# Optimization experiments

Measured on AMD Instinct MI355X. Metric: run time of the kernel, lower is better.

## Reference

```python
import jax, jax.numpy as jnp
import numpy as np

WS = 8      # window_size
NH = 8      # n_heads
EPS = 1e-06


def _rel_coords(ws):
    # Swin-style relative position index table, matches torch buffer construction
    c = np.stack(np.meshgrid(np.arange(ws), np.arange(ws), indexing='ij'))  # [2,ws,ws]
    c = c.reshape(2, -1)                      # [2, L]
    rel = c[:, :, None] - c[:, None, :]       # [2, L, L]
    rel = rel.transpose(1, 2, 0) + (ws - 1)   # [L, L, 2]
    rel[:, :, 0] *= 2 * ws - 1
    return jnp.asarray(rel.sum(-1), dtype=jnp.int32)  # [L, L]


def rms_film(x, t, gw, bw):
    # x: [B,C,H,W], t: [B,d_t]; RMS over channel dim, FiLM scale/shift from t
    g = (t @ gw.T)[:, :, None, None]
    b = (t @ bw.T)[:, :, None, None]
    return g * x * jax.lax.rsqrt(jnp.mean(x * x, axis=1, keepdims=True) + EPS) + b


def window_attn(x, wq, wk, wv, wo_w, wo_b, rpb):
    B, C, H, W = x.shape
    h, w = H // WS, W // WS
    L = WS * WS
    dh = C // NH
    # partition into windows: [B, h, w, L, C]
    xw = x.reshape(B, C, h, WS, w, WS).transpose(0, 2, 4, 3, 5, 1).reshape(B, h, w, L, C)

    def heads(p):
        y = xw @ p.T  # Linear, no bias
        return y.reshape(B, h, w, L, NH, dh).transpose(0, 1, 2, 4, 3, 5)  # [B,h,w,n,L,dh]

    q, k, v = heads(wq), heads(wk), heads(wv)
    bias = rpb[:, _rel_coords(WS)]  # [NH, L, L] gather from bias table
    attn = jnp.einsum('bhwnld,bhwnmd->bhwnlm', q, k) / float(np.sqrt(dh)) + bias
    o = jnp.einsum('bhwnlm,bhwnmd->bhwnld', jax.nn.softmax(attn, axis=-1), v)
    # merge windows, channel order (n c): [B, NH*dh, H, W]
    o = o.reshape(B, h, w, NH, WS, WS, dh).transpose(0, 3, 6, 1, 4, 2, 5).reshape(B, C, H, W)
    # 1x1 conv output projection (with bias)
    return jnp.einsum('bchw,oc->bohw', o, wo_w) + wo_b[None, :, None, None]


def convnext(x, t, dw_w, dw_b, gw, bw, w1, b1, w2, b2):
    # 7x7 depthwise conv, pad 3
    y = jax.lax.conv_general_dilated(
        x, dw_w, window_strides=(1, 1), padding=[(3, 3), (3, 3)],
        dimension_numbers=('NCHW', 'OIHW', 'NCHW'), feature_group_count=x.shape[1])
    y = y + dw_b[None, :, None, None]
    y = rms_film(y, t, gw, bw).transpose(0, 2, 3, 1)  # -> NHWC
    y = jax.nn.gelu(y @ w1.T + b1, approximate=False) @ w2.T + b2
    return y.transpose(0, 3, 1, 2)


def setup_inputs() -> dict:
    key = jax.random.key(0)
    ks = jax.random.split(key, 16)
    D, DT, B, H, W = 256, 256, 8, 128, 128
    DH = 4 * D
    n = lambda k, s: jax.random.normal(k, s, jnp.float32) * 0.02
    return dict(
        x=jax.random.normal(ks[0], (B, D, H, W), jnp.float32),
        t=jax.random.normal(ks[1], (B, DT), jnp.float32),
        an_g=n(ks[2], (D, DT)), an_b=n(ks[3], (D, DT)),
        wq=n(ks[4], (D, D)), wk=n(ks[5], (D, D)), wv=n(ks[6], (D, D)),
        wo_w=n(ks[7], (D, D)), wo_b=jnp.zeros((D,), jnp.float32),
        rpb=n(ks[8], (NH, (2 * WS - 1) ** 2)),
        dw_w=n(ks[9], (D, 1, 7, 7)), dw_b=jnp.zeros((D,), jnp.float32),
        fn_g=n(ks[10], (D, DT)), fn_b=n(ks[11], (D, DT)),
        w1=n(ks[12], (DH, D)), b1=jnp.zeros((DH,), jnp.float32),
        w2=n(ks[13], (D, DH)), b2=jnp.zeros((D,), jnp.float32))


def reference(x, t, an_g, an_b, wq, wk, wv, wo_w, wo_b, rpb,
              dw_w, dw_b, fn_g, fn_b, w1, b1, w2, b2):
    x = x + window_attn(rms_film(x, t, an_g, an_b), wq, wk, wv, wo_w, wo_b, rpb)
    return x + convnext(x, t, dw_w, dw_b, fn_g, fn_b, w1, b1, w2, b2)
```

## Files before the change

kernel.cpp:

```cpp
#include <hip/hip_runtime.h>
#include <math.h>

typedef __attribute__((ext_vector_type(8))) short bf16x8_t;
typedef __attribute__((ext_vector_type(4))) float f32x4;

__device__ __forceinline__ unsigned short f2bf(float f) {
  unsigned int u = __builtin_bit_cast(unsigned int, f);
  u += 0x7FFFu + ((u >> 16) & 1u);
  return (unsigned short)(u >> 16);
}
__device__ __forceinline__ float bf2f(unsigned short h) {
  unsigned int u = ((unsigned int)h) << 16;
  return __builtin_bit_cast(float, u);
}

typedef const __attribute__((address_space(1))) void* as1cv;
typedef __attribute__((address_space(3))) void* as3v;

__device__ __forceinline__ void gld_lds16(const unsigned short* g, unsigned short* l) {
  __builtin_amdgcn_global_load_lds((as1cv)g, (as3v)l, 16, 0, 0);
}

__global__ __launch_bounds__(256) void tvec_kernel(const float* __restrict__ t,
    const float* __restrict__ an_g, const float* __restrict__ an_b,
    const float* __restrict__ fn_g, const float* __restrict__ fn_b,
    float* __restrict__ gvec) {
  int d = threadIdx.x;
  int b = blockIdx.x;
  int m = blockIdx.y;
  __shared__ float ts[256];
  ts[d] = t[b * 256 + d];
  __syncthreads();
  const float* W = (m == 0) ? an_g : (m == 1) ? an_b : (m == 2) ? fn_g : fn_b;
  float acc = 0.f;
  #pragma unroll 8
  for (int k = 0; k < 256; ++k) acc += ts[k] * W[d * 256 + k];
  gvec[(m * 8 + b) * 256 + d] = acc;
}

__global__ __launch_bounds__(256) void wconv_kernel(const float* __restrict__ wq,
    const float* __restrict__ wk, const float* __restrict__ wv, const float* __restrict__ wo,
    const float* __restrict__ w1, const float* __restrict__ w2,
    unsigned short* __restrict__ outp) {
  int i = blockIdx.x * 256 + threadIdx.x;
  const float* src; int off;
  if      (i <  65536) { src = wq; off = 0; }
  else if (i < 131072) { src = wk; off = 65536; }
  else if (i < 196608) { src = wv; off = 131072; }
  else if (i < 262144) { src = wo; off = 196608; }
  else if (i < 524288) { src = w1; off = 262144; }
  else                 { src = w2; off = 524288; }
  outp[i] = f2bf(src[i - off]);
}

template<int IS_BF, int WX>
__global__ __launch_bounds__(256) void film_kernel(const void* __restrict__ in_,
    const float* __restrict__ gvec, int gsel, unsigned short* __restrict__ outbf,
    unsigned short* __restrict__ xbf) {
  const float* inf = (const float*)in_;
  const unsigned short* inb = (const unsigned short*)in_;
  int blk = blockIdx.x;
  int b = blk >> 8;
  int p0 = (blk & 255) << 6;
  int lane = threadIdx.x & 63;
  int cg = threadIdx.x >> 6;
  __shared__ unsigned short vals[64][264];
  __shared__ float ssred[4][64];
  __shared__ float rinvs[64];
  size_t base = ((size_t)b << 22) + p0;
  float ss = 0.f;
  #pragma unroll 4
  for (int ci = 0; ci < 64; ++ci) {
    int c = (cg << 6) + ci;
    size_t idx = base + ((size_t)c << 14) + lane;
    float v = IS_BF ? bf2f(inb[idx]) : inf[idx];
    ss += v * v;
    unsigned short hv = f2bf(v);
    vals[lane][c] = hv;
    if (WX) xbf[idx] = hv;
  }
  ssred[cg][lane] = ss;
  __syncthreads();
  if (threadIdx.x < 64) {
    float s = ssred[0][threadIdx.x] + ssred[1][threadIdx.x] + ssred[2][threadIdx.x] + ssred[3][threadIdx.x];
    rinvs[threadIdx.x] = rsqrtf(s * (1.0f / 256.0f) + 1e-6f);
  }
  __syncthreads();
  int pix = threadIdx.x >> 2;
  int c0 = (threadIdx.x & 3) << 6;
  float rv = rinvs[pix];
  const float* gp = gvec + ((gsel * 2 + 0) * 8 + b) * 256;
  const float* bp = gvec + ((gsel * 2 + 1) * 8 + b) * 256;
  unsigned short* orow = outbf + (((size_t)b << 14) + p0 + pix) * 256 + c0;
  #pragma unroll
  for (int ch = 0; ch < 8; ++ch) {
    bf16x8_t pack;
    #pragma unroll
    for (int e = 0; e < 8; ++e) {
      int c = c0 + ch * 8 + e;
      float v = bf2f(vals[pix][c]);
      float o = gp[c] * v * rv + bp[c];
      pack[e] = (short)f2bf(o);
    }
    *(bf16x8_t*)(orow + ch * 8) = pack;
  }
}

template<int DO_GELU>
__global__ __launch_bounds__(256) void gemm_kernel(const unsigned short* __restrict__ A,
    const unsigned short* __restrict__ Bw, const float* __restrict__ bias,
    unsigned short* __restrict__ outp, int K, int N) {
  __shared__ unsigned short As[128 * 64];
  __shared__ unsigned short Bs[128 * 64];
  int tid = threadIdx.x;
  int m0 = blockIdx.x << 7;
  int n0 = blockIdx.y << 7;
  int w = tid >> 6, lane = tid & 63;
  int wm = (w >> 1) << 6, wn = (w & 1) << 6;
  f32x4 acc[4][4];
  #pragma unroll
  for (int mi = 0; mi < 4; ++mi)
    #pragma unroll
    for (int ni = 0; ni < 4; ++ni)
      acc[mi][ni] = (f32x4){0.f, 0.f, 0.f, 0.f};

  for (int k0 = 0; k0 < K; k0 += 64) {
    #pragma unroll
    for (int r2 = 0; r2 < 4; ++r2) {
      int linear = (r2 << 8) + tid;
      int row = linear >> 3;
      int ch = linear & 7;
      gld_lds16(A  + (size_t)(m0 + row) * K + k0 + ch * 8, As + linear * 8);
      gld_lds16(Bw + (size_t)(n0 + row) * K + k0 + ch * 8, Bs + linear * 8);
    }
    __syncthreads();
    #pragma unroll
    for (int kk = 0; kk < 64; kk += 32) {
      bf16x8_t af[4], bq[4];
      int lr = lane & 15;
      int lk = ((lane >> 4) << 3) + kk;
      #pragma unroll
      for (int mi = 0; mi < 4; ++mi)
        af[mi] = *(const bf16x8_t*)(As + ((wm + (mi << 4) + lr) << 6) + lk);
      #pragma unroll
      for (int ni = 0; ni < 4; ++ni)
        bq[ni] = *(const bf16x8_t*)(Bs + ((wn + (ni << 4) + lr) << 6) + lk);
      #pragma unroll
      for (int mi = 0; mi < 4; ++mi)
        #pragma unroll
        for (int ni = 0; ni < 4; ++ni)
          acc[mi][ni] = __builtin_amdgcn_mfma_f32_16x16x32_bf16(af[mi], bq[ni], acc[mi][ni], 0, 0, 0);
    }
    __syncthreads();
  }
  int lr = lane & 15, lg = lane >> 4;
  #pragma unroll
  for (int mi = 0; mi < 4; ++mi) {
    #pragma unroll
    for (int ni = 0; ni < 4; ++ni) {
      int col = n0 + wn + (ni << 4) + lr;
      int row = m0 + wm + (mi << 4) + (lg << 2);
      f32x4 a = acc[mi][ni];
      #pragma unroll
      for (int i = 0; i < 4; ++i) {
        float v = a[i];
        if (DO_GELU) {
          v += bias[col];
          v = 0.5f * v * (1.0f + erff(v * 0.70710678118654752f));
        }
        outp[(size_t)(row + i) * N + col] = f2bf(v);
      }
    }
  }
}

__global__ __launch_bounds__(256) void gemm_t_kernel(const unsigned short* __restrict__ A,
    const unsigned short* __restrict__ Bw, unsigned short* __restrict__ outp) {
  __shared__ unsigned short smem[16384];
  unsigned short* As = smem;
  unsigned short* Bs = smem + 8192;
  const int K = 256;
  int tid = threadIdx.x;
  int m0 = blockIdx.x << 7;
  int n0 = blockIdx.y << 7;
  int w = tid >> 6, lane = tid & 63;
  int wm = (w >> 1) << 6, wn = (w & 1) << 6;
  f32x4 acc[4][4];
  #pragma unroll
  for (int mi = 0; mi < 4; ++mi)
    #pragma unroll
    for (int ni = 0; ni < 4; ++ni)
      acc[mi][ni] = (f32x4){0.f, 0.f, 0.f, 0.f};

  for (int k0 = 0; k0 < K; k0 += 64) {
    #pragma unroll
    for (int r2 = 0; r2 < 4; ++r2) {
      int linear = (r2 << 8) + tid;
      int row = linear >> 3;
      int ch = linear & 7;
      gld_lds16(A  + (size_t)(m0 + row) * K + k0 + ch * 8, As + linear * 8);
      gld_lds16(Bw + (size_t)(n0 + row) * K + k0 + ch * 8, Bs + linear * 8);
    }
    __syncthreads();
    #pragma unroll
    for (int kk = 0; kk < 64; kk += 32) {
      bf16x8_t af[4], bq[4];
      int lr = lane & 15;
      int lk = ((lane >> 4) << 3) + kk;
      #pragma unroll
      for (int mi = 0; mi < 4; ++mi)
        af[mi] = *(const bf16x8_t*)(As + ((wm + (mi << 4) + lr) << 6) + lk);
      #pragma unroll
      for (int ni = 0; ni < 4; ++ni)
        bq[ni] = *(const bf16x8_t*)(Bs + ((wn + (ni << 4) + lr) << 6) + lk);
      #pragma unroll
      for (int mi = 0; mi < 4; ++mi)
        #pragma unroll
        for (int ni = 0; ni < 4; ++ni)
          acc[mi][ni] = __builtin_amdgcn_mfma_f32_16x16x32_bf16(af[mi], bq[ni], acc[mi][ni], 0, 0, 0);
    }
    __syncthreads();
  }

  int lr = lane & 15, lg = lane >> 4;
  #pragma unroll
  for (int mi = 0; mi < 4; ++mi)
    #pragma unroll
    for (int ni = 0; ni < 4; ++ni) {
      int cl = wn + (ni << 4) + lr;
      int rl = wm + (mi << 4) + (lg << 2);
      f32x4 a = acc[mi][ni];
      #pragma unroll
      for (int i = 0; i < 4; ++i)
        smem[cl * 128 + rl + i] = f2bf(a[i]);
    }
  __syncthreads();

  int cl = tid >> 1;
  int half = tid & 1;
  int b = m0 >> 14;
  int pix = (m0 & 16383) + half * 64;
  int c = n0 + cl;
  const unsigned short* srow = smem + cl * 128 + half * 64;
  unsigned short* orow = outp + ((size_t)b * 256 + c) * 16384 + pix;
  #pragma unroll
  for (int jj = 0; jj < 8; ++jj)
    *(bf16x8_t*)(orow + jj * 8) = *(const bf16x8_t*)(srow + jj * 8);
}

__global__ __launch_bounds__(256) void gemm_wof_kernel(const unsigned short* __restrict__ A,
    const unsigned short* __restrict__ Bw, const float* __restrict__ bias,
    const unsigned short* __restrict__ xbf, unsigned short* __restrict__ outp) {
  __shared__ unsigned short smem[16384];
  unsigned short* As = smem;
  unsigned short* Bs = smem + 8192;
  const int K = 256;
  int tid = threadIdx.x;
  int m0 = blockIdx.x << 7;
  int n0 = blockIdx.y << 7;
  int w = tid >> 6, lane = tid & 63;
  int wm = (w >> 1) << 6, wn = (w & 1) << 6;
  f32x4 acc[4][4];
  #pragma unroll
  for (int mi = 0; mi < 4; ++mi)
    #pragma unroll
    for (int ni = 0; ni < 4; ++ni)
      acc[mi][ni] = (f32x4){0.f, 0.f, 0.f, 0.f};

  for (int k0 = 0; k0 < K; k0 += 64) {
    #pragma unroll
    for (int r2 = 0; r2 < 4; ++r2) {
      int linear = (r2 << 8) + tid;
      int row = linear >> 3;
      int ch = linear & 7;
      gld_lds16(A  + (size_t)(m0 + row) * K + k0 + ch * 8, As + linear * 8);
      gld_lds16(Bw + (size_t)(n0 + row) * K + k0 + ch * 8, Bs + linear * 8);
    }
    __syncthreads();
    #pragma unroll
    for (int kk = 0; kk < 64; kk += 32) {
      bf16x8_t af[4], bq[4];
      int lr = lane & 15;
      int lk = ((lane >> 4) << 3) + kk;
      #pragma unroll
      for (int mi = 0; mi < 4; ++mi)
        af[mi] = *(const bf16x8_t*)(As + ((wm + (mi << 4) + lr) << 6) + lk);
      #pragma unroll
      for (int ni = 0; ni < 4; ++ni)
        bq[ni] = *(const bf16x8_t*)(Bs + ((wn + (ni << 4) + lr) << 6) + lk);
      #pragma unroll
      for (int mi = 0; mi < 4; ++mi)
        #pragma unroll
        for (int ni = 0; ni < 4; ++ni)
          acc[mi][ni] = __builtin_amdgcn_mfma_f32_16x16x32_bf16(af[mi], bq[ni], acc[mi][ni], 0, 0, 0);
    }
    __syncthreads();
  }

  int lr = lane & 15, lg = lane >> 4;
  #pragma unroll
  for (int mi = 0; mi < 4; ++mi)
    #pragma unroll
    for (int ni = 0; ni < 4; ++ni) {
      int cl = wn + (ni << 4) + lr;
      int rl = wm + (mi << 4) + (lg << 2);
      f32x4 a = acc[mi][ni];
      #pragma unroll
      for (int i = 0; i < 4; ++i)
        smem[cl * 128 + rl + i] = f2bf(a[i]);
    }
  __syncthreads();

  int cl = tid >> 1;
  int half = tid & 1;
  int b = m0 >> 14;
  int pix = (m0 & 16383) + half * 64;
  int c = n0 + cl;
  const unsigned short* srow = smem + cl * 128 + half * 64;
  size_t gbase = ((size_t)b * 256 + c) * 16384 + pix;
  const unsigned short* xrow = xbf + gbase;
  unsigned short* orow = outp + gbase;
  float bb = bias[c];
  #pragma unroll
  for (int jj = 0; jj < 8; ++jj) {
    bf16x8_t sv = *(const bf16x8_t*)(srow + jj * 8);
    bf16x8_t xv = *(const bf16x8_t*)(xrow + jj * 8);
    bf16x8_t ov;
    #pragma unroll
    for (int e = 0; e < 8; ++e)
      ov[e] = (short)f2bf(bf2f((unsigned short)sv[e]) + bf2f((unsigned short)xv[e]) + bb);
    *(bf16x8_t*)(orow + jj * 8) = ov;
  }
}

__global__ __launch_bounds__(256, 3) void gemm_mlp_kernel(const unsigned short* __restrict__ z,
    const unsigned short* __restrict__ w1, const float* __restrict__ b1,
    const unsigned short* __restrict__ w2, const float* __restrict__ b2,
    const unsigned short* __restrict__ x1, float* __restrict__ outp) {
  __shared__ unsigned short ztile[64 * 256];
  __shared__ unsigned short hbuf[64 * 136];
  int tid = threadIdx.x;
  int m0 = blockIdx.x << 6;
  int w = tid >> 6, lane = tid & 63;
  int g = lane >> 4, lr = lane & 15;

  #pragma unroll
  for (int r2 = 0; r2 < 8; ++r2) {
    int linear = (r2 << 8) + tid;
    int row = linear >> 5;
    int ch = linear & 31;
    gld_lds16(z + (size_t)(m0 + row) * 256 + ((ch ^ (row & 7)) << 3), ztile + linear * 8);
  }
  __syncthreads();

  f32x4 acc[4][4];
  #pragma unroll
  for (int mi = 0; mi < 4; ++mi)
    #pragma unroll
    for (int ni = 0; ni < 4; ++ni)
      acc[mi][ni] = (f32x4){0.f, 0.f, 0.f, 0.f};

  #pragma unroll 1
  for (int j = 0; j < 8; ++j) {
    f32x4 hacc[4][2];
    #pragma unroll
    for (int mi = 0; mi < 4; ++mi) {
      hacc[mi][0] = (f32x4){0.f, 0.f, 0.f, 0.f};
      hacc[mi][1] = (f32x4){0.f, 0.f, 0.f, 0.f};
    }
    #pragma unroll
    for (int k32 = 0; k32 < 8; ++k32) {
      bf16x8_t af[4], bq[2];
      int cidx = (k32 << 2) + g;
      #pragma unroll
      for (int mi = 0; mi < 4; ++mi) {
        int row = mi * 16 + lr;
        af[mi] = *(const bf16x8_t*)(ztile + row * 256 + ((cidx ^ (row & 7)) << 3));
      }
      int kb = (k32 << 5) + (g << 3);
      #pragma unroll
      for (int ni = 0; ni < 2; ++ni)
        bq[ni] = *(const bf16x8_t*)(w1 + (size_t)(j * 128 + w * 32 + ni * 16 + lr) * 256 + kb);
      #pragma unroll
      for (int mi = 0; mi < 4; ++mi)
        #pragma unroll
        for (int ni = 0; ni < 2; ++ni)
          hacc[mi][ni] = __builtin_amdgcn_mfma_f32_16x16x32_bf16(af[mi], bq[ni], hacc[mi][ni], 0, 0, 0);
    }
    #pragma unroll
    for (int ni = 0; ni < 2; ++ni) {
      int hcol = w * 32 + ni * 16 + lr;
      float bb = b1[j * 128 + hcol];
      #pragma unroll
      for (int mi = 0; mi < 4; ++mi) {
        #pragma unroll
        for (int i = 0; i < 4; ++i) {
          float v = hacc[mi][ni][i] + bb;
          v = 0.5f * v * (1.0f + erff(v * 0.70710678118654752f));
          hbuf[(mi * 16 + g * 4 + i) * 136 + hcol] = f2bf(v);
        }
      }
    }
    __syncthreads();
    #pragma unroll
    for (int ks = 0; ks < 4; ++ks) {
      int kb = (ks << 5) + (g << 3);
      bf16x8_t pf[4], bq2[4];
      #pragma unroll
      for (int mi = 0; mi < 4; ++mi)
        pf[mi] = *(const bf16x8_t*)(hbuf + (mi * 16 + lr) * 136 + kb);
      #pragma unroll
      for (int ni = 0; ni < 4; ++ni)
        bq2[ni] = *(const bf16x8_t*)(w2 + (size_t)(w * 64 + ni * 16 + lr) * 1024 + j * 128 + kb);
      #pragma unroll
      for (int mi = 0; mi < 4; ++mi)
        #pragma unroll
        for (int ni = 0; ni < 4; ++ni)
          acc[mi][ni] = __builtin_amdgcn_mfma_f32_16x16x32_bf16(pf[mi], bq2[ni], acc[mi][ni], 0, 0, 0);
    }
    __syncthreads();
  }

  unsigned short* stg = ztile;
  #pragma unroll
  for (int mi = 0; mi < 4; ++mi)
    #pragma unroll
    for (int ni = 0; ni < 4; ++ni) {
      int cl = w * 64 + ni * 16 + lr;
      int rl = mi * 16 + g * 4;
      f32x4 a = acc[mi][ni];
      #pragma unroll
      for (int i = 0; i < 4; ++i)
        stg[cl * 64 + ((rl + i) ^ ((cl & 7) << 3))] = f2bf(a[i]);
    }
  __syncthreads();
  int c = tid;
  int b = m0 >> 14;
  int pix = m0 & 16383;
  size_t gbase = ((size_t)b * 256 + c) * 16384 + pix;
  const unsigned short* xrow = x1 + gbase;
  float* orow = outp + gbase;
  float bb = b2[c];
  #pragma unroll
  for (int jj = 0; jj < 8; ++jj) {
    bf16x8_t sv = *(const bf16x8_t*)(stg + c * 64 + ((jj ^ (c & 7)) << 3));
    bf16x8_t xv = *(const bf16x8_t*)(xrow + jj * 8);
    #pragma unroll
    for (int e = 0; e < 8; ++e)
      orow[jj * 8 + e] = bf2f((unsigned short)sv[e]) + bf2f((unsigned short)xv[e]) + bb;
  }
}

__global__ __launch_bounds__(256, 4) void attn_kernel(const unsigned short* __restrict__ qg,
    const unsigned short* __restrict__ kg, const unsigned short* __restrict__ vt,
    const float* __restrict__ rpb, unsigned short* __restrict__ og) {
  __shared__ float rpbf[1800];
  __shared__ unsigned short pbuf[4][16 * 72];
  int wi = (blockIdx.x & 7) * 256 + (blockIdx.x >> 3);
  int b = wi >> 8, wh = (wi >> 4) & 15, ww = wi & 15;
  int tid = threadIdx.x;
  int w = tid >> 6, lane = tid & 63;
  int g = lane >> 4, lr = lane & 15;
  for (int idx = tid; idx < 1800; idx += 256) rpbf[idx] = rpb[idx];
  __syncthreads();

  int rowpix = (wh * 8) * 128 + ww * 8;
  size_t ibase = ((size_t)b << 14) + rowpix;
  unsigned short* pb = pbuf[w];
  const float scale = 0.17677669529663689f;

  #pragma unroll 1
  for (int hh = 0; hh < 2; ++hh) {
    int h = w * 2 + hh;
    bf16x8_t qf[4], kf[4];
    #pragma unroll
    for (int t = 0; t < 4; ++t) {
      size_t tok = ibase + (size_t)(t * 2 + (lr >> 3)) * 128 + (lr & 7);
      qf[t] = *(const bf16x8_t*)(qg + tok * 256 + h * 32 + g * 8);
      kf[t] = *(const bf16x8_t*)(kg + tok * 256 + h * 32 + g * 8);
    }
    bf16x8_t vfr[2][2];
    #pragma unroll
    for (int ks = 0; ks < 2; ++ks)
      #pragma unroll
      for (int dt = 0; dt < 2; ++dt) {
        size_t plane = (size_t)b * 256 + h * 32 + dt * 16 + lr;
        vfr[ks][dt] = *(const bf16x8_t*)(vt + (plane << 14) + rowpix + (size_t)(ks * 4 + g) * 128);
      }
    const float* rb = &rpbf[h * 225];

    #pragma unroll 1
    for (int qt = 0; qt < 4; ++qt) {
      f32x4 sacc[4];
      #pragma unroll
      for (int kt = 0; kt < 4; ++kt)
        sacc[kt] = __builtin_amdgcn_mfma_f32_16x16x32_bf16(qf[qt], kf[kt],
                     (f32x4){0.f, 0.f, 0.f, 0.f}, 0, 0, 0);
      float sums[4];
      #pragma unroll
      for (int i = 0; i < 4; ++i) {
        int q = qt * 16 + g * 4 + i;
        int il = q >> 3, jl = q & 7;
        float v[4];
        #pragma unroll
        for (int kt = 0; kt < 4; ++kt) {
          int kv = kt * 16 + lr;
          v[kt] = sacc[kt][i] * scale + rb[(il - (kv >> 3) + 7) * 15 + (jl - (kv & 7) + 7)];
        }
        float mx = fmaxf(fmaxf(v[0], v[1]), fmaxf(v[2], v[3]));
        mx = fmaxf(mx, __shfl_xor(mx, 1));
        mx = fmaxf(mx, __shfl_xor(mx, 2));
        mx = fmaxf(mx, __shfl_xor(mx, 4));
        mx = fmaxf(mx, __shfl_xor(mx, 8));
        float sm = 0.f;
        #pragma unroll
        for (int kt = 0; kt < 4; ++kt) { v[kt] = __expf(v[kt] - mx); sm += v[kt]; }
        sm += __shfl_xor(sm, 1);
        sm += __shfl_xor(sm, 2);
        sm += __shfl_xor(sm, 4);
        sm += __shfl_xor(sm, 8);
        sums[i] = sm;
        #pragma unroll
        for (int kt = 0; kt < 4; ++kt)
          pb[(g * 4 + i) * 72 + kt * 16 + lr] = f2bf(v[kt]);
      }
      f32x4 oacc[2] = {(f32x4){0.f, 0.f, 0.f, 0.f}, (f32x4){0.f, 0.f, 0.f, 0.f}};
      #pragma unroll
      for (int ks = 0; ks < 2; ++ks) {
        bf16x8_t pf = *(const bf16x8_t*)(pb + lr * 72 + ks * 32 + g * 8);
        oacc[0] = __builtin_amdgcn_mfma_f32_16x16x32_bf16(pf, vfr[ks][0], oacc[0], 0, 0, 0);
        oacc[1] = __builtin_amdgcn_mfma_f32_16x16x32_bf16(pf, vfr[ks][1], oacc[1], 0, 0, 0);
      }
      #pragma unroll
      for (int i = 0; i < 4; ++i) {
        int q = qt * 16 + g * 4 + i;
        float inv = 1.0f / sums[i];
        size_t tok = ibase + (size_t)(q >> 3) * 128 + (q & 7);
        og[tok * 256 + h * 32 + lr] = f2bf(oacc[0][i] * inv);
        og[tok * 256 + h * 32 + 16 + lr] = f2bf(oacc[1][i] * inv);
      }
    }
  }
}

__global__ __launch_bounds__(256) void dwconv_kernel(const unsigned short* __restrict__ x1,
    const float* __restrict__ w, const float* __restrict__ bias, unsigned short* __restrict__ outp) {
  int bc = blockIdx.y;
  int c = bc & 255;
  int y0 = blockIdx.x << 6;
  __shared__ unsigned short tile[70 * 144];
  __shared__ float wf[49];
  const unsigned short* plane = x1 + ((size_t)bc << 14);
  int tid = threadIdx.x;

  for (int idx = tid; idx < 70 * 16; idx += 256) {
    int row = idx >> 4, ch = idx & 15;
    int gy = y0 - 3 + row;
    bf16x8_t v = (bf16x8_t){0, 0, 0, 0, 0, 0, 0, 0};
    if (gy >= 0 && gy < 128) v = *(const bf16x8_t*)(plane + gy * 128 + ch * 8);
    *(bf16x8_t*)(&tile[row * 144 + 8 + ch * 8]) = v;
  }
  for (int idx = tid; idx < 70 * 6; idx += 256) {
    int row = idx / 6, e = idx % 6;
    int col = (e < 3) ? (5 + e) : (133 + e);
    tile[row * 144 + col] = 0;
  }
  if (tid < 49) wf[tid] = w[c * 49 + tid];
  __syncthreads();

  int r = tid >> 2;
  int c0 = (tid & 3) << 5;
  float acc[32];
  float bb = bias[c];
  #pragma unroll
  for (int i = 0; i < 32; ++i) acc[i] = bb;

  #pragma unroll
  for (int u = 0; u < 7; ++u) {
    const unsigned short* rowp = &tile[(r + u) * 144 + c0];
    float f[48];
    #pragma unroll
    for (int k = 0; k < 6; ++k) {
      bf16x8_t v = *(const bf16x8_t*)(rowp + k * 8);
      #pragma unroll
      for (int e = 0; e < 8; ++e) f[k * 8 + e] = bf2f((unsigned short)v[e]);
    }
    #pragma unroll
    for (int t = 0; t < 7; ++t) {
      float wv = wf[u * 7 + t];
      #pragma unroll
      for (int i = 0; i < 32; ++i) acc[i] += f[i + 5 + t] * wv;
    }
  }

  unsigned short* orow = outp + ((size_t)bc << 14) + (size_t)(y0 + r) * 128 + c0;
  #pragma unroll
  for (int k = 0; k < 4; ++k) {
    bf16x8_t v;
    #pragma unroll
    for (int e = 0; e < 8; ++e) v[e] = (short)f2bf(acc[k * 8 + e]);
    *(bf16x8_t*)(orow + k * 8) = v;
  }
}

extern "C" void kernel_launch(void* const* d_in, const int* in_sizes, int n_in,
                              void* d_out, int out_size, void* d_ws, size_t ws_size,
                              hipStream_t stream) {
  const float* x    = (const float*)d_in[0];
  const float* t    = (const float*)d_in[1];
  const float* an_g = (const float*)d_in[2];
  const float* an_b = (const float*)d_in[3];
  const float* wq   = (const float*)d_in[4];
  const float* wk   = (const float*)d_in[5];
  const float* wv   = (const float*)d_in[6];
  const float* wo_w = (const float*)d_in[7];
  const float* wo_b = (const float*)d_in[8];
  const float* rpb  = (const float*)d_in[9];
  const float* dw_w = (const float*)d_in[10];
  const float* dw_b = (const float*)d_in[11];
  const float* fn_g = (const float*)d_in[12];
  const float* fn_b = (const float*)d_in[13];
  const float* w1   = (const float*)d_in[14];
  const float* b1   = (const float*)d_in[15];
  const float* w2   = (const float*)d_in[16];
  const float* b2   = (const float*)d_in[17];
  float* outp = (float*)d_out;

  char* ws = (char*)d_ws;
  const size_t MB = 1024ull * 1024ull;
  float* gvec = (float*)ws;
  unsigned short* wbf = (unsigned short*)(ws + 32768);
  unsigned short* P = (unsigned short*)(ws + 2 * MB);
  unsigned short* Q = (unsigned short*)(ws + 66 * MB);
  unsigned short* R = (unsigned short*)(ws + 130 * MB);
  unsigned short* xbf  = (unsigned short*)d_out;
  unsigned short* vbuf = (unsigned short*)((char*)d_out + 64 * MB);

  unsigned short* wq_bf = wbf;
  unsigned short* wk_bf = wbf + 65536;
  unsigned short* wv_bf = wbf + 131072;
  unsigned short* wo_bf = wbf + 196608;
  unsigned short* w1_bf = wbf + 262144;
  unsigned short* w2_bf = wbf + 524288;

  tvec_kernel<<<dim3(8, 4), 256, 0, stream>>>(t, an_g, an_b, fn_g, fn_b, gvec);
  wconv_kernel<<<3072, 256, 0, stream>>>(wq, wk, wv, wo_w, w1, w2, wbf);

  film_kernel<0, 1><<<2048, 256, 0, stream>>>(x, gvec, 0, P, xbf);

  gemm_kernel<0><<<dim3(1024, 2), 256, 0, stream>>>(P, wq_bf, nullptr, Q, 256, 256);
  gemm_kernel<0><<<dim3(1024, 2), 256, 0, stream>>>(P, wk_bf, nullptr, R, 256, 256);
  gemm_t_kernel<<<dim3(1024, 2), 256, 0, stream>>>(P, wv_bf, vbuf);

  attn_kernel<<<2048, 256, 0, stream>>>(Q, R, vbuf, rpb, P);

  gemm_wof_kernel<<<dim3(1024, 2), 256, 0, stream>>>(P, wo_bf, wo_b, xbf, R);

  dwconv_kernel<<<dim3(2, 2048), 256, 0, stream>>>(R, dw_w, dw_b, Q);
  film_kernel<1, 0><<<2048, 256, 0, stream>>>(Q, gvec, 1, P, nullptr);

  gemm_mlp_kernel<<<2048, 256, 0, stream>>>(P, w1_bf, b1, w2_bf, b2, R, outp);
}
```

Before: 891.9 us.

## Split fused MLP GEMM across 8 waves with double-buffered hidden tile

The fused MLP kernel now runs 512 threads (8 waves) per block instead of 4. Each wave computes half as many hidden columns and output channels, which cuts accumulator registers and lets more waves hide latency. The hidden-activation LDS buffer is double-buffered so the trailing barrier per chunk can be dropped. The cost is more LDS per block and more redundant LDS reads of the shared z tile per wave.

```diff
diff --git a/kernel.cpp b/kernel.cpp
--- a/kernel.cpp
+++ b/kernel.cpp
@@ -333,71 +333,63 @@
   }
 }
 
-__global__ __launch_bounds__(256, 3) void gemm_mlp_kernel(const unsigned short* __restrict__ z,
+__global__ __launch_bounds__(512, 4) void gemm_mlp_kernel(const unsigned short* __restrict__ z,
     const unsigned short* __restrict__ w1, const float* __restrict__ b1,
     const unsigned short* __restrict__ w2, const float* __restrict__ b2,
     const unsigned short* __restrict__ x1, float* __restrict__ outp) {
   __shared__ unsigned short ztile[64 * 256];
-  __shared__ unsigned short hbuf[64 * 136];
+  __shared__ unsigned short hbuf[2][64 * 136];
   int tid = threadIdx.x;
   int m0 = blockIdx.x << 6;
   int w = tid >> 6, lane = tid & 63;
   int g = lane >> 4, lr = lane & 15;
 
   #pragma unroll
-  for (int r2 = 0; r2 < 8; ++r2) {
-    int linear = (r2 << 8) + tid;
+  for (int r2 = 0; r2 < 4; ++r2) {
+    int linear = (r2 << 9) + tid;
     int row = linear >> 5;
     int ch = linear & 31;
     gld_lds16(z + (size_t)(m0 + row) * 256 + ((ch ^ (row & 7)) << 3), ztile + linear * 8);
   }
   __syncthreads();
 
-  f32x4 acc[4][4];
-  #pragma unroll
-  for (int mi = 0; mi < 4; ++mi)
-    #pragma unroll
-    for (int ni = 0; ni < 4; ++ni)
-      acc[mi][ni] = (f32x4){0.f, 0.f, 0.f, 0.f};
+  f32x4 acc[4][2];
+  #pragma unroll
+  for (int mi = 0; mi < 4; ++mi) {
+    acc[mi][0] = (f32x4){0.f, 0.f, 0.f, 0.f};
+    acc[mi][1] = (f32x4){0.f, 0.f, 0.f, 0.f};
+  }
 
   #pragma unroll 1
   for (int j = 0; j < 8; ++j) {
-    f32x4 hacc[4][2];
-    #pragma unroll
-    for (int mi = 0; mi < 4; ++mi) {
-      hacc[mi][0] = (f32x4){0.f, 0.f, 0.f, 0.f};
-      hacc[mi][1] = (f32x4){0.f, 0.f, 0.f, 0.f};
-    }
+    f32x4 hacc[4];
+    #pragma unroll
+    for (int mi = 0; mi < 4; ++mi) hacc[mi] = (f32x4){0.f, 0.f, 0.f, 0.f};
     #pragma unroll
     for (int k32 = 0; k32 < 8; ++k32) {
-      bf16x8_t af[4], bq[2];
       int cidx = (k32 << 2) + g;
+      bf16x8_t af[4];
       #pragma unroll
       for (int mi = 0; mi < 4; ++mi) {
         int row = mi * 16 + lr;
         af[mi] = *(const bf16x8_t*)(ztile + row * 256 + ((cidx ^ (row & 7)) << 3));
       }
-      int kb = (k32 << 5) + (g << 3);
-      #pragma unroll
-      for (int ni = 0; ni < 2; ++ni)
-        bq[ni] = *(const bf16x8_t*)(w1 + (size_t)(j * 128 + w * 32 + ni * 16 + lr) * 256 + kb);
-      #pragma unroll
-      for (int mi = 0; mi < 4; ++mi)
-        #pragma unroll
-        for (int ni = 0; ni < 2; ++ni)
-          hacc[mi][ni] = __builtin_amdgcn_mfma_f32_16x16x32_bf16(af[mi], bq[ni], hacc[mi][ni], 0, 0, 0);
-    }
-    #pragma unroll
-    for (int ni = 0; ni < 2; ++ni) {
-      int hcol = w * 32 + ni * 16 + lr;
+      bf16x8_t bq = *(const bf16x8_t*)(w1 + (size_t)(j * 128 + w * 16 + lr) * 256 + (k32 << 5) + (g << 3));
+      #pragma unroll
+      for (int mi = 0; mi < 4; ++mi)
+        hacc[mi] = __builtin_amdgcn_mfma_f32_16x16x32_bf16(af[mi], bq, hacc[mi], 0, 0, 0);
+    }
+    unsigned short* hb = hbuf[j & 1];
+    {
+      int hcol = w * 16 + lr;
       float bb = b1[j * 128 + hcol];
       #pragma unroll
       for (int mi = 0; mi < 4; ++mi) {
         #pragma unroll
         for (int i = 0; i < 4; ++i) {
-          float v = hacc[mi][ni][i] + bb;
+          float v = hacc[mi][i] + bb;
           v = 0.5f * v * (1.0f + erff(v * 0.70710678118654752f));
-          hbuf[(mi * 16 + g * 4 + i) * 136 + hcol] = f2bf(v);
+          hb[(mi * 16 + g * 4 + i) * 136 + hcol] = f2bf(v);
         }
       }
     }
@@ -405,28 +397,27 @@
     #pragma unroll
     for (int ks = 0; ks < 4; ++ks) {
       int kb = (ks << 5) + (g << 3);
-      bf16x8_t pf[4], bq2[4];
-      #pragma unroll
-      for (int mi = 0; mi < 4; ++mi)
-        pf[mi] = *(const bf16x8_t*)(hbuf + (mi * 16 + lr) * 136 + kb);
-      #pragma unroll
-      for (int ni = 0; ni < 4; ++ni)
-        bq2[ni] = *(const bf16x8_t*)(w2 + (size_t)(w * 64 + ni * 16 + lr) * 1024 + j * 128 + kb);
-      #pragma unroll
-      for (int mi = 0; mi < 4; ++mi)
-        #pragma unroll
-        for (int ni = 0; ni < 4; ++ni)
+      bf16x8_t pf[4], bq2[2];
+      #pragma unroll
+      for (int mi = 0; mi < 4; ++mi)
+        pf[mi] = *(const bf16x8_t*)(hb + (mi * 16 + lr) * 136 + kb);
+      #pragma unroll
+      for (int ni = 0; ni < 2; ++ni)
+        bq2[ni] = *(const bf16x8_t*)(w2 + (size_t)(w * 32 + ni * 16 + lr) * 1024 + j * 128 + kb);
+      #pragma unroll
+      for (int mi = 0; mi < 4; ++mi)
+        #pragma unroll
+        for (int ni = 0; ni < 2; ++ni)
           acc[mi][ni] = __builtin_amdgcn_mfma_f32_16x16x32_bf16(pf[mi], bq2[ni], acc[mi][ni], 0, 0, 0);
     }
-    __syncthreads();
   }
 
   unsigned short* stg = ztile;
   #pragma unroll
   for (int mi = 0; mi < 4; ++mi)
     #pragma unroll
-    for (int ni = 0; ni < 4; ++ni) {
-      int cl = w * 64 + ni * 16 + lr;
+    for (int ni = 0; ni < 2; ++ni) {
+      int cl = w * 32 + ni * 16 + lr;
       int rl = mi * 16 + g * 4;
       f32x4 a = acc[mi][ni];
       #pragma unroll
@@ -434,20 +425,22 @@
         stg[cl * 64 + ((rl + i) ^ ((cl & 7) << 3))] = f2bf(a[i]);
     }
   __syncthreads();
-  int c = tid;
+  int c = tid >> 1;
+  int half = tid & 1;
   int b = m0 >> 14;
-  int pix = m0 & 16383;
-  size_t gbase = ((size_t)b * 256 + c) * 16384 + pix;
+  int pix0 = (m0 & 16383) + half * 32;
+  size_t gbase = ((size_t)b * 256 + c) * 16384 + pix0;
   const unsigned short* xrow = x1 + gbase;
   float* orow = outp + gbase;
   float bb = b2[c];
   #pragma unroll
-  for (int jj = 0; jj < 8; ++jj) {
+  for (int jj2 = 0; jj2 < 4; ++jj2) {
+    int jj = half * 4 + jj2;
     bf16x8_t sv = *(const bf16x8_t*)(stg + c * 64 + ((jj ^ (c & 7)) << 3));
-    bf16x8_t xv = *(const bf16x8_t*)(xrow + jj * 8);
+    bf16x8_t xv = *(const bf16x8_t*)(xrow + jj2 * 8);
     #pragma unroll
     for (int e = 0; e < 8; ++e)
-      orow[jj * 8 + e] = bf2f((unsigned short)sv[e]) + bf2f((unsigned short)xv[e]) + bb;
+      orow[jj2 * 8 + e] = bf2f((unsigned short)sv[e]) + bf2f((unsigned short)xv[e]) + bb;
   }
 }
 
@@ -659,5 +652,5 @@
   dwconv_kernel<<<dim3(2, 2048), 256, 0, stream>>>(R, dw_w, dw_b, Q);
   film_kernel<1, 0><<<2048, 256, 0, stream>>>(Q, gvec, 1, P, nullptr);
 
-  gemm_mlp_kernel<<<2048, 256, 0, stream>>>(P, w1_bf, b1, w2_bf, b2, R, outp);
-}
+  gemm_mlp_kernel<<<2048, 512, 0, stream>>>(P, w1_bf, b1, w2_bf, b2, R, outp);
+}
```

Result: faster. 838.1 us (-6.0%).
